# Performance work log

Measured on AMD Instinct MI355X. Metric: run time of the kernel, lower is better.

## Reference

```python
import jax, jax.numpy as jnp
import numpy as np

EPS = 1e-4  # module eps for normalized()


def _conv(x, w, b):
    # 3x3 conv, stride 1, padding 1 (SAME), NCHW/OIHW
    y = jax.lax.conv_general_dilated(x, w, (1, 1), 'SAME',
                                     dimension_numbers=('NCHW', 'OIHW', 'NCHW'))
    return y + b[None, :, None, None]


def _normalized(x, eps):
    return x / (jnp.sqrt(jnp.sum(x * x, axis=1, keepdims=True)) + eps)


def setup_inputs() -> dict:
    key = jax.random.key(0)
    ks = iter(jax.random.split(key, 40))
    B, H, W = 1024, 20, 20
    D = {}
    D['s'] = jax.random.randint(next(ks), (B, H, W), 0, 14, dtype=jnp.int32)
    D['s_prime'] = jax.random.randint(next(ks), (B, H, W), 0, 14, dtype=jnp.int32)
    D['downscale_factor'] = 1
    def rn(shape, scale=0.05):
        return (jax.random.normal(next(ks), shape, dtype=jnp.float32) * scale)
    D['emb_table'] = rn((14, 8), 1.0)
    D['ec0_w'], D['ec0_b'] = rn((32, 8, 3, 3)), rn((32,))
    D['ec1_w'], D['ec1_b'] = rn((64, 32, 3, 3)), rn((64,))
    for p in ('p1', 'p2', 'p3'):
        D[p + 'c0_w'], D[p + 'c0_b'] = rn((64, 64, 3, 3)), rn((64,))
        D[p + 'c1_w'], D[p + 'c1_b'] = rn((128, 64, 3, 3)), rn((128,))
        D[p + 'l_w'], D[p + 'l_b'] = rn((512, 51200), 0.01), rn((512,))
    D['fc0_w'], D['fc0_b'] = rn((512, 512)), rn((512,))
    D['fc1_w'], D['fc1_b'] = rn((512, 512)), rn((512,))
    D['p3f0_w'], D['p3f0_b'] = rn((512, 512)), rn((512,))
    D['p3f1_w'], D['p3f1_b'] = rn((512, 512)), rn((512,))
    D['z_vec'] = rn((64, 512), 1.0)
    D['scale'] = jnp.zeros((1,), dtype=jnp.float32)
    return D


def _forward(s, s_prime, downscale_factor, emb_table,
             ec0_w, ec0_b, ec1_w, ec1_b,
             p1c0_w, p1c0_b, p1c1_w, p1c1_b, p1l_w, p1l_b,
             p2c0_w, p2c0_b, p2c1_w, p2c1_b, p2l_w, p2l_b,
             p3c0_w, p3c0_b, p3c1_w, p3c1_b, p3l_w, p3l_b,
             fc0_w, fc0_b, fc1_w, fc1_b,
             p3f0_w, p3f0_b, p3f1_w, p3f1_b,
             z_vec, scale):
    relu = jax.nn.relu
    # nn.Embedding(max_norm=1): renorm rows with L2 norm > 1 (torch uses +1e-7)
    norms = jnp.linalg.norm(emb_table, axis=1, keepdims=True)
    tbl = emb_table * jnp.where(norms > 1.0, 1.0 / (norms + 1e-7), 1.0)

    def embed(idx):
        x = tbl[idx]                      # [B,H,W,E]
        x = jnp.transpose(x, (0, 3, 1, 2))  # [B,E,H,W]
        x = relu(_conv(x, ec0_w, ec0_b))
        x = relu(_conv(x, ec1_w, ec1_b))  # last_activation=True
        return x

    def phi(x, c0w, c0b, c1w, c1b, lw, lb):
        x = relu(_conv(x, c0w, c0b))
        x = relu(_conv(x, c1w, c1b))      # last_activation=True
        x = x.reshape(x.shape[0], -1)     # torch.flatten(start_dim=1), CHW order
        return x @ lw.T + lb

    s_embed = embed(s)
    sp_embed = embed(s_prime)
    s_int = phi(s_embed, p1c0_w, p1c0_b, p1c1_w, p1c1_b, p1l_w, p1l_b)
    diff_int = phi(sp_embed - s_embed, p2c0_w, p2c0_b, p2c1_w, p2c1_b, p2l_w, p2l_b)
    # phi3: conv stack + linear + fc stack (no last relu) + normalize(eps)
    h3 = phi(sp_embed, p3c0_w, p3c0_b, p3c1_w, p3c1_b, p3l_w, p3l_b)
    h3 = relu(h3 @ p3f0_w.T + p3f0_b)
    h3 = h3 @ p3f1_w.T + p3f1_b
    sp_out = _normalized(h3, EPS)

    # quantize: cdist(x, z) then argmax (as in source), gather codebook rows
    d2 = (jnp.sum(diff_int * diff_int, axis=1, keepdims=True)
          + jnp.sum(z_vec * z_vec, axis=1)[None, :]
          - 2.0 * diff_int @ z_vec.T)
    dist = jnp.sqrt(jnp.maximum(d2, 0.0))
    z_inds = jnp.argmax(dist, axis=1)
    z_matrix = z_vec[z_inds]

    # fc path (source forward adds the quantize result to s_intermediate)
    h = s_int + z_matrix
    h = relu(h @ fc0_w.T + fc0_b)
    h = h @ fc1_w.T + fc1_b
    s_out = _normalized(h, EPS)

    if downscale_factor == 1:
        ipm = s_out @ sp_out.T
    else:
        bs = s_out.shape[0] // downscale_factor
        E = s_out.shape[1]
        v1 = s_out[::downscale_factor].reshape(bs, 1, E)
        v2 = sp_out.reshape(bs, downscale_factor, E)
        ipm = jnp.einsum('bie,bje->bj', v1, v2)
    return jnp.exp(scale) * ipm


def reference(s, s_prime, downscale_factor, emb_table,
              ec0_w, ec0_b, ec1_w, ec1_b,
              p1c0_w, p1c0_b, p1c1_w, p1c1_b, p1l_w, p1l_b,
              p2c0_w, p2c0_b, p2c1_w, p2c1_b, p2l_w, p2l_b,
              p3c0_w, p3c0_b, p3c1_w, p3c1_b, p3l_w, p3l_b,
              fc0_w, fc0_b, fc1_w, fc1_b,
              p3f0_w, p3f0_b, p3f1_w, p3f1_b,
              z_vec, scale):
    return _forward(s, s_prime, downscale_factor, emb_table,
                    ec0_w, ec0_b, ec1_w, ec1_b,
                    p1c0_w, p1c0_b, p1c1_w, p1c1_b, p1l_w, p1l_b,
                    p2c0_w, p2c0_b, p2c1_w, p2c1_b, p2l_w, p2l_b,
                    p3c0_w, p3c0_b, p3c1_w, p3c1_b, p3l_w, p3l_b,
                    fc0_w, fc0_b, fc1_w, fc1_b,
                    p3f0_w, p3f0_b, p3f1_w, p3f1_b,
                    z_vec, scale)
```

## Files before the change

### kernel.cpp

```cpp
#include <hip/hip_runtime.h>
#include <cstddef>


typedef _Float16 f16;
typedef _Float16 f16x8 __attribute__((ext_vector_type(8)));
typedef _Float16 f16x4 __attribute__((ext_vector_type(4)));
typedef float f32x4 __attribute__((ext_vector_type(4)));

struct ConvArgs {
  const f16* in0[3];
  const f16* in1[3];
  const f16* wr[3];
  const float* bias[3];
  f16* out[3];
};

struct WROrd {
  const float* w[3];
  f16* o[3];
  int COUT, CIN, KPAD;
};

struct GemmArgs {
  const float* X[3];
  const float* W[3];
  const float* B[3];
  float* Y[3];
  int K, N, relu;
  const float* scale;
};

__global__ void renorm_k(const float* __restrict__ emb, f16* __restrict__ tbl) {
  int t = threadIdx.x;
  if (t < 14) {
    float s = 0.f;
    for (int e = 0; e < 8; ++e) { float v = emb[t * 8 + e]; s += v * v; }
    float n = sqrtf(s);
    float sc = (n > 1.0f) ? 1.0f / (n + 1e-7f) : 1.0f;
    for (int e = 0; e < 8; ++e) tbl[t * 8 + e] = (f16)(emb[t * 8 + e] * sc);
  }
}

__global__ __launch_bounds__(256) void wreorder_k(WROrd a) {
  int i = blockIdx.x * 256 + threadIdx.x;
  int z = blockIdx.z;
  if (i >= a.COUT * a.KPAD) return;
  int co = i / a.KPAD, k = i % a.KPAD;
  int tap = k / a.CIN, cin = k % a.CIN;
  float v = (tap < 9) ? a.w[z][((size_t)co * a.CIN + cin) * 9 + tap] : 0.f;
  a.o[z][i] = (f16)v;
}

__global__ __launch_bounds__(256) void gather_k(
    const int* __restrict__ s, const int* __restrict__ sp,
    const f16* __restrict__ tbl, f16* __restrict__ o_s, f16* __restrict__ o_sp,
    int start) {
  int i = blockIdx.x * 256 + threadIdx.x;
  int bp = start * 400 + i;
  uint4 rs = ((const uint4*)tbl)[s[bp]];
  uint4 rp = ((const uint4*)tbl)[sp[bp]];
  ((uint4*)o_s)[i] = rs;
  ((uint4*)o_sp)[i] = rp;
}

template <int CIN, int CINC, int COT, bool NCHW_OUT, int OC, int KPAD>
__global__ __launch_bounds__(256) void conv_mfma_k(ConvArgs args) {
  constexpr int TPS = 32 / CINC;
  constexpr int KSTEPS = (9 + TPS - 1) / TPS;
  constexpr int WROW = KSTEPS * 32 + 8;
  constexpr int CS = (CINC == 32) ? 40 : (CINC == 16 ? 24 : 8);
  constexpr int NT = COT / 16;
  constexpr int NCH = CIN / CINC;
  constexpr int GPP = CINC / 8;

  const int b = blockIdx.x;
  const int cobase = blockIdx.y * COT;
  const int z = blockIdx.z;
  const f16* __restrict__ in0 = args.in0[z];
  const f16* __restrict__ in1 = args.in1[z];
  const f16* __restrict__ wr = args.wr[z];
  const float* __restrict__ bias = args.bias[z];
  f16* __restrict__ out = args.out[z];

  __shared__ f16 in_lds[484 * CS];
  __shared__ f16 w_lds[COT * WROW];

  const int tid = threadIdx.x;
  const int lane = tid & 63;
  const int wv = tid >> 6;
  const int l15 = lane & 15;
  const int quad = lane >> 4;

  int qbase[7];
#pragma unroll
  for (int i = 0; i < 7; ++i) {
    int mt = wv + 4 * i;
    int p = mt * 16 + l15;
    if (p > 399) p = 399;
    qbase[i] = (p / 20 + 1) * 22 + (p % 20 + 1);
  }

  f32x4 acc[7][NT];
#pragma unroll
  for (int i = 0; i < 7; ++i)
#pragma unroll
    for (int n = 0; n < NT; ++n) acc[i][n] = (f32x4){0.f, 0.f, 0.f, 0.f};

  for (int cc = 0; cc < NCH; ++cc) {
    __syncthreads();
    for (int l = tid; l < 484 * GPP; l += 256) {
      int pp = l / GPP, g = l % GPP;
      int hp = pp / 22, wp = pp % 22;
      f16x8 v = {0, 0, 0, 0, 0, 0, 0, 0};
      if (hp >= 1 && hp <= 20 && wp >= 1 && wp <= 20) {
        int p = (hp - 1) * 20 + (wp - 1);
        size_t gi = ((size_t)b * 400 + p) * CIN + cc * CINC + g * 8;
        v = *(const f16x8*)(in0 + gi);
        if (in1) v = v - *(const f16x8*)(in1 + gi);
      }
      *(f16x8*)(&in_lds[pp * CS + g * 8]) = v;
    }
    for (int l = tid; l < COT * KSTEPS * 4; l += 256) {
      int co = l / (KSTEPS * 4);
      int rem = l % (KSTEPS * 4);
      int s2 = rem >> 2, g = rem & 3;
      int tap, src;
      if (GPP == 4)      { tap = s2;               src = s2 * CIN + cc * 32 + g * 8; }
      else if (GPP == 2) { tap = s2 * 2 + (g >> 1); src = tap * CIN + cc * 16 + (g & 1) * 8; }
      else               { tap = s2 * 4 + g;        src = s2 * 32 + g * 8; }
      f16x8 wv8 = {0, 0, 0, 0, 0, 0, 0, 0};
      if (GPP == 1 || tap < 9)
        wv8 = *(const f16x8*)(&wr[(size_t)(cobase + co) * KPAD + src]);
      *(f16x8*)(&w_lds[co * WROW + s2 * 32 + g * 8]) = wv8;
    }
    __syncthreads();

#pragma unroll
    for (int s = 0; s < KSTEPS; ++s) {
      f16x8 bf[NT];
#pragma unroll
      for (int n = 0; n < NT; ++n)
        bf[n] = *(const f16x8*)(&w_lds[(n * 16 + l15) * WROW + s * 32 + quad * 8]);
      int tap = (GPP == 4) ? s : (GPP == 2 ? s * 2 + (quad >> 1) : s * 4 + quad);
      if (tap > 8) tap = 8;
      int toff = (tap / 3 - 1) * 22 + (tap % 3 - 1);
      int coff = (GPP == 4) ? quad * 8 : (GPP == 2 ? (quad & 1) * 8 : 0);
#pragma unroll
      for (int i = 0; i < 7; ++i) {
        f16x8 af = *(const f16x8*)(&in_lds[(qbase[i] + toff) * CS + coff]);
#pragma unroll
        for (int n = 0; n < NT; ++n)
          acc[i][n] = __builtin_amdgcn_mfma_f32_16x16x32_f16(af, bf[n], acc[i][n], 0, 0, 0);
      }
    }
  }

#pragma unroll
  for (int i = 0; i < 7; ++i) {
    int mt = wv + 4 * i;
    if (mt >= 25) continue;
#pragma unroll
    for (int n = 0; n < NT; ++n) {
      int co = cobase + n * 16 + l15;
      float bv = bias[co];
      if (NCHW_OUT) {
        f16x4 pk;
#pragma unroll
        for (int r = 0; r < 4; ++r)
          pk[r] = (f16)fmaxf(acc[i][n][r] + bv, 0.f);
        *(f16x4*)(&out[(size_t)b * (400 * OC) + (size_t)co * 400 + mt * 16 + quad * 4]) = pk;
      } else {
#pragma unroll
        for (int r = 0; r < 4; ++r) {
          int pix = mt * 16 + quad * 4 + r;
          out[((size_t)b * 400 + pix) * OC + co] =
              (f16)fmaxf(acc[i][n][r] + bv, 0.f);
        }
      }
    }
  }
}

__global__ __launch_bounds__(256) void gemm_big_k(
    const f16* __restrict__ X, const float* __restrict__ W,
    float* __restrict__ Y) {
  const int m0 = blockIdx.x * 128, n0 = blockIdx.y * 128;
  const int kb = blockIdx.z * 2560;
  __shared__ f16 Xs[128 * 40];
  __shared__ f16 Ws[128 * 40];

  const int tid = threadIdx.x;
  const int lane = tid & 63, wv = tid >> 6;
  const int l15 = lane & 15, quad = lane >> 4;
  const int wm = (wv >> 1) * 64, wn = (wv & 1) * 64;
  const int srow = tid >> 1, shalf = tid & 1;

  f32x4 acc[4][4];
#pragma unroll
  for (int i = 0; i < 4; ++i)
#pragma unroll
    for (int j = 0; j < 4; ++j) acc[i][j] = (f32x4){0.f, 0.f, 0.f, 0.f};

  const f16* xg = X + (size_t)(m0 + srow) * 51200 + kb + shalf * 16;
  const float* wg = W + (size_t)(n0 + srow) * 51200 + kb + shalf * 16;

  for (int k0 = 0; k0 < 2560; k0 += 32) {
    f16x8 x0 = *(const f16x8*)(xg + k0);
    f16x8 x1 = *(const f16x8*)(xg + k0 + 8);
    float4 w0 = *(const float4*)(wg + k0);
    float4 w1 = *(const float4*)(wg + k0 + 4);
    float4 w2 = *(const float4*)(wg + k0 + 8);
    float4 w3 = *(const float4*)(wg + k0 + 12);
    __syncthreads();
    *(f16x8*)(&Xs[srow * 40 + shalf * 16]) = x0;
    *(f16x8*)(&Xs[srow * 40 + shalf * 16 + 8]) = x1;
    f16x8 wa = {(f16)w0.x, (f16)w0.y, (f16)w0.z, (f16)w0.w,
                (f16)w1.x, (f16)w1.y, (f16)w1.z, (f16)w1.w};
    f16x8 wb = {(f16)w2.x, (f16)w2.y, (f16)w2.z, (f16)w2.w,
                (f16)w3.x, (f16)w3.y, (f16)w3.z, (f16)w3.w};
    *(f16x8*)(&Ws[srow * 40 + shalf * 16]) = wa;
    *(f16x8*)(&Ws[srow * 40 + shalf * 16 + 8]) = wb;
    __syncthreads();
    f16x8 a[4], bfr[4];
#pragma unroll
    for (int t = 0; t < 4; ++t) {
      a[t] = *(const f16x8*)(&Xs[(wm + t * 16 + l15) * 40 + quad * 8]);
      bfr[t] = *(const f16x8*)(&Ws[(wn + t * 16 + l15) * 40 + quad * 8]);
    }
#pragma unroll
    for (int mt = 0; mt < 4; ++mt)
#pragma unroll
      for (int nt = 0; nt < 4; ++nt)
        acc[mt][nt] = __builtin_amdgcn_mfma_f32_16x16x32_f16(a[mt], bfr[nt], acc[mt][nt], 0, 0, 0);
  }

#pragma unroll
  for (int mt = 0; mt < 4; ++mt)
#pragma unroll
    for (int nt = 0; nt < 4; ++nt) {
      int row = m0 + wm + mt * 16 + quad * 4;
      int col = n0 + wn + nt * 16 + l15;
#pragma unroll
      for (int r = 0; r < 4; ++r)
        atomicAdd(&Y[(size_t)(row + r) * 512 + col], acc[mt][nt][r]);
    }
}

__global__ __launch_bounds__(256) void initlin_k(
    float* l0, float* l1, float* l2,
    const float* b0, const float* b1, const float* b2) {
  int i = blockIdx.x * 256 + threadIdx.x;
  float* Y = blockIdx.y == 0 ? l0 : (blockIdx.y == 1 ? l1 : l2);
  const float* B = blockIdx.y == 0 ? b0 : (blockIdx.y == 1 ? b1 : b2);
  Y[i] = B[i & 511];
}

__global__ __launch_bounds__(256) void gemm_xwT_k(GemmArgs g) {
  const int z = blockIdx.z;
  const float* __restrict__ X = g.X[z];
  const float* __restrict__ W = g.W[z];
  const float* __restrict__ Bi = g.B[z];
  float* __restrict__ Y = g.Y[z];
  const int K = g.K, N = g.N;
  const int m0 = blockIdx.x * 64, n0 = blockIdx.y * 64;
  __shared__ float Xs[16][68];
  __shared__ float Ws[16][68];
  const int tid = threadIdx.x;
  const int tm = tid & 15, tn = tid >> 4;
  const int lr = tid >> 2, lc = (tid & 3) << 2;
  float acc[4][4];
#pragma unroll
  for (int i = 0; i < 4; ++i)
#pragma unroll
    for (int j = 0; j < 4; ++j) acc[i][j] = 0.f;
  const float* xg = X + (size_t)(m0 + lr) * K + lc;
  const float* wg = W + (size_t)(n0 + lr) * K + lc;
  for (int k0 = 0; k0 < K; k0 += 16) {
    float4 xv = *(const float4*)(xg + k0);
    float4 wv = *(const float4*)(wg + k0);
    __syncthreads();
    Xs[lc + 0][lr] = xv.x; Xs[lc + 1][lr] = xv.y;
    Xs[lc + 2][lr] = xv.z; Xs[lc + 3][lr] = xv.w;
    Ws[lc + 0][lr] = wv.x; Ws[lc + 1][lr] = wv.y;
    Ws[lc + 2][lr] = wv.z; Ws[lc + 3][lr] = wv.w;
    __syncthreads();
#pragma unroll
    for (int k = 0; k < 16; ++k) {
      float4 a = *(const float4*)(&Xs[k][tm << 2]);
      float4 bv = *(const float4*)(&Ws[k][tn << 2]);
      acc[0][0] = fmaf(a.x, bv.x, acc[0][0]); acc[0][1] = fmaf(a.x, bv.y, acc[0][1]);
      acc[0][2] = fmaf(a.x, bv.z, acc[0][2]); acc[0][3] = fmaf(a.x, bv.w, acc[0][3]);
      acc[1][0] = fmaf(a.y, bv.x, acc[1][0]); acc[1][1] = fmaf(a.y, bv.y, acc[1][1]);
      acc[1][2] = fmaf(a.y, bv.z, acc[1][2]); acc[1][3] = fmaf(a.y, bv.w, acc[1][3]);
      acc[2][0] = fmaf(a.z, bv.x, acc[2][0]); acc[2][1] = fmaf(a.z, bv.y, acc[2][1]);
      acc[2][2] = fmaf(a.z, bv.z, acc[2][2]); acc[2][3] = fmaf(a.z, bv.w, acc[2][3]);
      acc[3][0] = fmaf(a.w, bv.x, acc[3][0]); acc[3][1] = fmaf(a.w, bv.y, acc[3][1]);
      acc[3][2] = fmaf(a.w, bv.z, acc[3][2]); acc[3][3] = fmaf(a.w, bv.w, acc[3][3]);
    }
  }
  float alpha = 1.0f;
  if (g.scale) alpha = expf(g.scale[0]);
#pragma unroll
  for (int i = 0; i < 4; ++i) {
    size_t row = (size_t)(m0 + tm * 4 + i) * N + n0;
#pragma unroll
    for (int j = 0; j < 4; ++j) {
      float v = acc[i][j];
      if (Bi) v += Bi[n0 + tn * 4 + j];
      if (g.relu) v = fmaxf(v, 0.f);
      Y[row + tn * 4 + j] = v * alpha;
    }
  }
}

__global__ __launch_bounds__(256) void quantize_k(
    const float* __restrict__ diff_int, const float* __restrict__ s_int,
    const float* __restrict__ z_vec, float* __restrict__ hq) {
  const int wv = threadIdx.x >> 6, lane = threadIdx.x & 63;
  const int row = blockIdx.x * 4 + wv;
  const float* d = diff_int + (size_t)row * 512;
  const float* zr = z_vec + (size_t)lane * 512;
  float dot = 0.f, zz = 0.f;
  for (int k = 0; k < 512; k += 4) {
    float4 dv = *(const float4*)(d + k);
    float4 zv = *(const float4*)(zr + k);
    dot = fmaf(dv.x, zv.x, dot); dot = fmaf(dv.y, zv.y, dot);
    dot = fmaf(dv.z, zv.z, dot); dot = fmaf(dv.w, zv.w, dot);
    zz = fmaf(zv.x, zv.x, zz); zz = fmaf(zv.y, zv.y, zz);
    zz = fmaf(zv.z, zv.z, zz); zz = fmaf(zv.w, zv.w, zz);
  }
  float gval = zz - 2.0f * dot;
  int best = lane;
  float bg = gval;
#pragma unroll
  for (int off = 32; off; off >>= 1) {
    float og = __shfl_xor(bg, off);
    int ob = __shfl_xor(best, off);
    if (og > bg || (og == bg && ob < best)) { bg = og; best = ob; }
  }
  const float* zb = z_vec + (size_t)best * 512;
  const float* si = s_int + (size_t)row * 512;
  float* o = hq + (size_t)row * 512;
  for (int k = lane; k < 512; k += 64) o[k] = si[k] + zb[k];
}

__global__ __launch_bounds__(256) void normalize_k(
    const float* __restrict__ v0, const float* __restrict__ v1,
    float* __restrict__ o0, float* __restrict__ o1) {
  const int wv = threadIdx.x >> 6, lane = threadIdx.x & 63;
  const int row = blockIdx.x * 4 + wv;
  const float* x = (blockIdx.y ? v1 : v0) + (size_t)row * 512;
  float* o = (blockIdx.y ? o1 : o0) + (size_t)row * 512;
  float vals[8];
  float ss = 0.f;
#pragma unroll
  for (int k = 0; k < 8; ++k) {
    vals[k] = x[lane + 64 * k];
    ss = fmaf(vals[k], vals[k], ss);
  }
#pragma unroll
  for (int off = 32; off; off >>= 1) ss += __shfl_xor(ss, off);
  float inv = 1.0f / (sqrtf(ss) + 1e-4f);
#pragma unroll
  for (int k = 0; k < 8; ++k) o[lane + 64 * k] = vals[k] * inv;
}

extern "C" void kernel_launch(void* const* d_in, const int* in_sizes, int n_in,
                              void* d_out, int out_size, void* d_ws, size_t ws_size,
                              hipStream_t stream) {
  (void)in_sizes; (void)n_in; (void)out_size;
  const int* s  = (const int*)d_in[0];
  const int* sp = (const int*)d_in[1];
  const float* emb   = (const float*)d_in[3];
  const float* ec0_w = (const float*)d_in[4];
  const float* ec0_b = (const float*)d_in[5];
  const float* ec1_w = (const float*)d_in[6];
  const float* ec1_b = (const float*)d_in[7];
  const float* pc0_w[3] = {(const float*)d_in[8],  (const float*)d_in[14], (const float*)d_in[20]};
  const float* pc0_b[3] = {(const float*)d_in[9],  (const float*)d_in[15], (const float*)d_in[21]};
  const float* pc1_w[3] = {(const float*)d_in[10], (const float*)d_in[16], (const float*)d_in[22]};
  const float* pc1_b[3] = {(const float*)d_in[11], (const float*)d_in[17], (const float*)d_in[23]};
  const float* pl_w[3]  = {(const float*)d_in[12], (const float*)d_in[18], (const float*)d_in[24]};
  const float* pl_b[3]  = {(const float*)d_in[13], (const float*)d_in[19], (const float*)d_in[25]};
  const float* fc0_w  = (const float*)d_in[26];
  const float* fc0_b  = (const float*)d_in[27];
  const float* fc1_w  = (const float*)d_in[28];
  const float* fc1_b  = (const float*)d_in[29];
  const float* p3f0_w = (const float*)d_in[30];
  const float* p3f0_b = (const float*)d_in[31];
  const float* p3f1_w = (const float*)d_in[32];
  const float* p3f1_b = (const float*)d_in[33];
  const float* z_vec  = (const float*)d_in[34];
  const float* scale  = (const float*)d_in[35];
  float* outp = (float*)d_out;

  float* ws = (float*)d_ws;
  float* lin0 = ws;
  float* lin1 = lin0 + 524288;
  float* lin2 = lin1 + 524288;
  float* hq   = lin2 + 524288;
  float* u0   = hq + 524288;
  float* u1   = u0 + 524288;
  float* v0   = u1 + 524288;
  float* v1   = v0 + 524288;
  float* so   = v1 + 524288;
  float* spo  = so + 524288;
  f16* hbase  = (f16*)(ws + 10 * 524288);
  f16* tbl_h   = hbase;
  f16* wr_ec0  = hbase + 128;
  f16* wr_ec1  = wr_ec0 + 3072;
  f16* wr_pc0  = wr_ec1 + 18432;
  f16* wr_pc1  = wr_pc0 + 110592;
  f16* chunk0  = wr_pc1 + 221184;

  const size_t FIXED = (size_t)(10 * 524288) * 4 + (size_t)(128 + 3072 + 18432 + 110592 + 221184) * 2;
  int C = 1024;
  while (C > 128) {
    if (FIXED + (size_t)C * 256000 <= ws_size) break;
    C >>= 1;
  }
  const int NCHUNK = 1024 / C;

  f16* emb_s  = chunk0;
  f16* emb_sp = emb_s + (size_t)C * 25600;
  f16* t0     = emb_sp + (size_t)C * 25600;
  f16* t1     = t0 + (size_t)C * 25600;
  f16* x8_s   = t1;
  f16* x8_sp  = x8_s + (size_t)C * 3200;
  f16* a32_s  = x8_sp + (size_t)C * 3200;
  f16* a32_sp = a32_s + (size_t)C * 12800;

  renorm_k<<<1, 64, 0, stream>>>(emb, tbl_h);
  {
    WROrd a{}; a.w[0] = ec0_w; a.o[0] = wr_ec0; a.COUT = 32; a.CIN = 8; a.KPAD = 96;
    wreorder_k<<<dim3(12, 1, 1), 256, 0, stream>>>(a);
  }
  {
    WROrd a{}; a.w[0] = ec1_w; a.o[0] = wr_ec1; a.COUT = 64; a.CIN = 32; a.KPAD = 288;
    wreorder_k<<<dim3(72, 1, 1), 256, 0, stream>>>(a);
  }
  {
    WROrd a{};
    for (int p = 0; p < 3; ++p) { a.w[p] = pc0_w[p]; a.o[p] = wr_pc0 + (size_t)p * 36864; }
    a.COUT = 64; a.CIN = 64; a.KPAD = 576;
    wreorder_k<<<dim3(144, 1, 3), 256, 0, stream>>>(a);
  }
  {
    WROrd a{};
    for (int p = 0; p < 3; ++p) { a.w[p] = pc1_w[p]; a.o[p] = wr_pc1 + (size_t)p * 73728; }
    a.COUT = 128; a.CIN = 64; a.KPAD = 576;
    wreorder_k<<<dim3(288, 1, 3), 256, 0, stream>>>(a);
  }
  initlin_k<<<dim3(2048, 3), 256, 0, stream>>>(lin0, lin1, lin2,
                                               pl_b[0], pl_b[1], pl_b[2]);

  for (int ch = 0; ch < NCHUNK; ++ch) {
    const int start = ch * C;
    gather_k<<<C * 400 / 256, 256, 0, stream>>>(s, sp, tbl_h, x8_s, x8_sp, start);
    {
      ConvArgs a{};
      a.in0[0] = x8_s;  a.wr[0] = wr_ec0; a.bias[0] = ec0_b; a.out[0] = a32_s;
      a.in0[1] = x8_sp; a.wr[1] = wr_ec0; a.bias[1] = ec0_b; a.out[1] = a32_sp;
      conv_mfma_k<8, 8, 32, false, 32, 96><<<dim3(C, 1, 2), 256, 0, stream>>>(a);
    }
    {
      ConvArgs a{};
      a.in0[0] = a32_s;  a.wr[0] = wr_ec1; a.bias[0] = ec1_b; a.out[0] = emb_s;
      a.in0[1] = a32_sp; a.wr[1] = wr_ec1; a.bias[1] = ec1_b; a.out[1] = emb_sp;
      conv_mfma_k<32, 16, 64, false, 64, 288><<<dim3(C, 1, 2), 256, 0, stream>>>(a);
    }
    for (int p = 0; p < 3; ++p) {
      {
        ConvArgs a{};
        a.in0[0] = (p == 0) ? emb_s : emb_sp;
        a.in1[0] = (p == 1) ? emb_s : nullptr;
        a.wr[0] = wr_pc0 + (size_t)p * 36864; a.bias[0] = pc0_b[p]; a.out[0] = t0;
        conv_mfma_k<64, 16, 64, false, 64, 576><<<dim3(C, 1, 1), 256, 0, stream>>>(a);
      }
      {
        ConvArgs a{};
        a.in0[0] = t0;
        a.wr[0] = wr_pc1 + (size_t)p * 73728; a.bias[0] = pc1_b[p]; a.out[0] = t1;
        conv_mfma_k<64, 16, 64, true, 128, 576><<<dim3(C, 2, 1), 256, 0, stream>>>(a);
      }
      float* lin = (p == 0) ? lin0 : (p == 1) ? lin1 : lin2;
      gemm_big_k<<<dim3(C / 128, 4, 20), 256, 0, stream>>>(
          t1, pl_w[p], lin + (size_t)start * 512);
    }
  }

  quantize_k<<<256, 256, 0, stream>>>(lin1, lin0, z_vec, hq);
  {
    GemmArgs g{};
    g.X[0] = hq;   g.W[0] = fc0_w;  g.B[0] = fc0_b;  g.Y[0] = u0;
    g.X[1] = lin2; g.W[1] = p3f0_w; g.B[1] = p3f0_b; g.Y[1] = u1;
    g.K = 512; g.N = 512; g.relu = 1; g.scale = nullptr;
    gemm_xwT_k<<<dim3(16, 8, 2), 256, 0, stream>>>(g);
  }
  {
    GemmArgs g{};
    g.X[0] = u0; g.W[0] = fc1_w;  g.B[0] = fc1_b;  g.Y[0] = v0;
    g.X[1] = u1; g.W[1] = p3f1_w; g.B[1] = p3f1_b; g.Y[1] = v1;
    g.K = 512; g.N = 512; g.relu = 0; g.scale = nullptr;
    gemm_xwT_k<<<dim3(16, 8, 2), 256, 0, stream>>>(g);
  }
  normalize_k<<<dim3(256, 2), 256, 0, stream>>>(v0, v1, so, spo);
  {
    GemmArgs g{};
    g.X[0] = so; g.W[0] = spo; g.B[0] = nullptr; g.Y[0] = outp;
    g.K = 512; g.N = 1024; g.relu = 0; g.scale = scale;
    gemm_xwT_k<<<dim3(16, 16, 1), 256, 0, stream>>>(g);
  }
}
```

Before: 1.884 ms.

## Pre-swizzle big linear weights to fp16 K-blocked layout and load MFMA fragments directly

Adds a pass that converts the three 512x51200 fp32 linear weights into fp16 laid out in 32-wide K blocks, and makes the conv producing the linear input write the same K-blocked layout. The big GEMM then loads MFMA fragments straight from global memory without LDS staging or barriers, and the K split is tuned to the chunk size. This halves weight bytes read per chunk and removes the shared-memory round trip. In exchange it adds a 157 MB fp16 workspace plus a conversion pass each call, and uncoalesced-ish direct global fragment loads with no LDS reuse between waves.

```diff
diff --git a/kernel.cpp b/kernel.cpp
--- a/kernel.cpp
+++ b/kernel.cpp
@@ -13,12 +13,18 @@
   const f16* wr[3];
   const float* bias[3];
   f16* out[3];
+  int xm;
 };
 
 struct WROrd {
   const float* w[3];
   f16* o[3];
   int COUT, CIN, KPAD;
+};
+
+struct WswzArgs {
+  const float* w[3];
+  f16* o[3];
 };
 
 struct GemmArgs {
@@ -49,6 +55,18 @@
   int tap = k / a.CIN, cin = k % a.CIN;
   float v = (tap < 9) ? a.w[z][((size_t)co * a.CIN + cin) * 9 + tap] : 0.f;
   a.o[z][i] = (f16)v;
+}
+
+__global__ __launch_bounds__(256) void wswz_k(WswzArgs a) {
+  int i = blockIdx.x * 256 + threadIdx.x;
+  const float* __restrict__ W = a.w[blockIdx.z];
+  f16* __restrict__ O = a.o[blockIdx.z];
+  int n = i / 6400, kg = (i % 6400) * 8;
+  float4 x0 = *(const float4*)(W + (size_t)n * 51200 + kg);
+  float4 x1 = *(const float4*)(W + (size_t)n * 51200 + kg + 4);
+  f16x8 v = {(f16)x0.x, (f16)x0.y, (f16)x0.z, (f16)x0.w,
+             (f16)x1.x, (f16)x1.y, (f16)x1.z, (f16)x1.w};
+  *(f16x8*)(&O[((size_t)(kg >> 5) * 512 + n) * 32 + (kg & 31)]) = v;
 }
 
 __global__ __launch_bounds__(256) void gather_k(
@@ -164,11 +182,12 @@
       int co = cobase + n * 16 + l15;
       float bv = bias[co];
       if (NCHW_OUT) {
+        int k = co * 400 + mt * 16 + quad * 4;
         f16x4 pk;
 #pragma unroll
         for (int r = 0; r < 4; ++r)
           pk[r] = (f16)fmaxf(acc[i][n][r] + bv, 0.f);
-        *(f16x4*)(&out[(size_t)b * (400 * OC) + (size_t)co * 400 + mt * 16 + quad * 4]) = pk;
+        *(f16x4*)(&out[((size_t)(k >> 5) * args.xm + b) * 32 + (k & 31)]) = pk;
       } else {
 #pragma unroll
         for (int r = 0; r < 4; ++r) {
@@ -182,18 +201,12 @@
 }
 
 __global__ __launch_bounds__(256) void gemm_big_k(
-    const f16* __restrict__ X, const float* __restrict__ W,
-    float* __restrict__ Y) {
+    const f16* __restrict__ Xp, const f16* __restrict__ Wp,
+    float* __restrict__ Y, int XM, int kslice) {
   const int m0 = blockIdx.x * 128, n0 = blockIdx.y * 128;
-  const int kb = blockIdx.z * 2560;
-  __shared__ f16 Xs[128 * 40];
-  __shared__ f16 Ws[128 * 40];
-
-  const int tid = threadIdx.x;
-  const int lane = tid & 63, wv = tid >> 6;
+  const int lane = threadIdx.x & 63, wv = threadIdx.x >> 6;
   const int l15 = lane & 15, quad = lane >> 4;
   const int wm = (wv >> 1) * 64, wn = (wv & 1) * 64;
-  const int srow = tid >> 1, shalf = tid & 1;
 
   f32x4 acc[4][4];
 #pragma unroll
@@ -201,31 +214,20 @@
 #pragma unroll
     for (int j = 0; j < 4; ++j) acc[i][j] = (f32x4){0.f, 0.f, 0.f, 0.f};
 
-  const f16* xg = X + (size_t)(m0 + srow) * 51200 + kb + shalf * 16;
-  const float* wg = W + (size_t)(n0 + srow) * 51200 + kb + shalf * 16;
-
-  for (int k0 = 0; k0 < 2560; k0 += 32) {
-    f16x8 x0 = *(const f16x8*)(xg + k0);
-    f16x8 x1 = *(const f16x8*)(xg + k0 + 8);
-    float4 w0 = *(const float4*)(wg + k0);
-    float4 w1 = *(const float4*)(wg + k0 + 4);
-    float4 w2 = *(const float4*)(wg + k0 + 8);
-    float4 w3 = *(const float4*)(wg + k0 + 12);
-    __syncthreads();
-    *(f16x8*)(&Xs[srow * 40 + shalf * 16]) = x0;
-    *(f16x8*)(&Xs[srow * 40 + shalf * 16 + 8]) = x1;
-    f16x8 wa = {(f16)w0.x, (f16)w0.y, (f16)w0.z, (f16)w0.w,
-                (f16)w1.x, (f16)w1.y, (f16)w1.z, (f16)w1.w};
-    f16x8 wb = {(f16)w2.x, (f16)w2.y, (f16)w2.z, (f16)w2.w,
-                (f16)w3.x, (f16)w3.y, (f16)w3.z, (f16)w3.w};
-    *(f16x8*)(&Ws[srow * 40 + shalf * 16]) = wa;
-    *(f16x8*)(&Ws[srow * 40 + shalf * 16 + 8]) = wb;
-    __syncthreads();
+  const int kb0 = (blockIdx.z * kslice) >> 5;
+  const f16* xb = Xp + ((size_t)kb0 * XM + (m0 + wm + l15)) * 32 + quad * 8;
+  const f16* wb = Wp + ((size_t)kb0 * 512 + (n0 + wn + l15)) * 32 + quad * 8;
+  const size_t xstep = (size_t)XM * 32;
+  const size_t wstep = 512 * 32;
+  const int iters = kslice >> 5;
+
+#pragma unroll 2
+  for (int kk = 0; kk < iters; ++kk) {
     f16x8 a[4], bfr[4];
 #pragma unroll
     for (int t = 0; t < 4; ++t) {
-      a[t] = *(const f16x8*)(&Xs[(wm + t * 16 + l15) * 40 + quad * 8]);
-      bfr[t] = *(const f16x8*)(&Ws[(wn + t * 16 + l15) * 40 + quad * 8]);
+      a[t] = *(const f16x8*)(xb + (size_t)kk * xstep + t * 512);
+      bfr[t] = *(const f16x8*)(wb + (size_t)kk * wstep + t * 512);
     }
 #pragma unroll
     for (int mt = 0; mt < 4; ++mt)
@@ -411,15 +413,19 @@
   f16* wr_ec1  = wr_ec0 + 3072;
   f16* wr_pc0  = wr_ec1 + 18432;
   f16* wr_pc1  = wr_pc0 + 110592;
-  f16* chunk0  = wr_pc1 + 221184;
-
-  const size_t FIXED = (size_t)(10 * 524288) * 4 + (size_t)(128 + 3072 + 18432 + 110592 + 221184) * 2;
+  f16* wp_big  = wr_pc1 + 221184;
+  f16* chunk0  = wp_big + 78643200;
+
+  const size_t FIXED = (size_t)(10 * 524288) * 4 +
+                       (size_t)(128 + 3072 + 18432 + 110592 + 221184 + 78643200) * 2;
   int C = 1024;
   while (C > 128) {
     if (FIXED + (size_t)C * 256000 <= ws_size) break;
     C >>= 1;
   }
   const int NCHUNK = 1024 / C;
+  const int KS = (C == 1024) ? 16 : (C == 512) ? 32 : (C == 256) ? 64 : 100;
+  const int kslice = 51200 / KS;
 
   f16* emb_s  = chunk0;
   f16* emb_sp = emb_s + (size_t)C * 25600;
@@ -450,6 +456,11 @@
     for (int p = 0; p < 3; ++p) { a.w[p] = pc1_w[p]; a.o[p] = wr_pc1 + (size_t)p * 73728; }
     a.COUT = 128; a.CIN = 64; a.KPAD = 576;
     wreorder_k<<<dim3(288, 1, 3), 256, 0, stream>>>(a);
+  }
+  {
+    WswzArgs a{};
+    for (int p = 0; p < 3; ++p) { a.w[p] = pl_w[p]; a.o[p] = wp_big + (size_t)p * 26214400; }
+    wswz_k<<<dim3(12800, 1, 3), 256, 0, stream>>>(a);
   }
   initlin_k<<<dim3(2048, 3), 256, 0, stream>>>(lin0, lin1, lin2,
                                                pl_b[0], pl_b[1], pl_b[2]);
@@ -481,11 +492,12 @@
         ConvArgs a{};
         a.in0[0] = t0;
         a.wr[0] = wr_pc1 + (size_t)p * 73728; a.bias[0] = pc1_b[p]; a.out[0] = t1;
+        a.xm = C;
         conv_mfma_k<64, 16, 64, true, 128, 576><<<dim3(C, 2, 1), 256, 0, stream>>>(a);
       }
       float* lin = (p == 0) ? lin0 : (p == 1) ? lin1 : lin2;
-      gemm_big_k<<<dim3(C / 128, 4, 20), 256, 0, stream>>>(
-          t1, pl_w[p], lin + (size_t)start * 512);
+      gemm_big_k<<<dim3(C / 128, 4, KS), 256, 0, stream>>>(
+          t1, wp_big + (size_t)p * 26214400, lin + (size_t)start * 512, C, kslice);
     }
   }
 
```

New measurement: 1.934 ms. +2.7%, slower.
